# Performance work log

Measured on AMD Instinct MI355X. Metric: run time of the kernel, lower is better.

Reference implementation:

```python
import jax, jax.numpy as jnp
import numpy as np

B, P, N, E, IN, HID, NL, MULT = 4, 8, 2000, 2000, 16, 128, 3, 4
LOGIT_CLIP = 10.0

def setup_inputs() -> dict:
    key = jax.random.key(0)
    ks = jax.random.split(key, 8)
    s = 0.05
    return {
        "node_features": jax.random.normal(ks[0], (B, P, N, IN), jnp.float32),
        "incidence": jax.random.uniform(ks[1], (B, N, E), jnp.float32),  # weighted incidence
        "W_in": s * jax.random.normal(ks[2], (IN, HID), jnp.float32),
        "edge_Ws": s * jax.random.normal(ks[3], (NL, HID, HID), jnp.float32),
        "node_Ws": s * jax.random.normal(ks[4], (NL, HID, HID), jnp.float32),
        "W1": s * jax.random.normal(ks[5], (HID, MULT * HID), jnp.float32),
        "W2": s * jax.random.normal(ks[6], (MULT * HID, HID), jnp.float32),
        "W_dec": s * jax.random.normal(ks[7], (HID, 1), jnp.float32),
    }

def reference(node_features, incidence, W_in, edge_Ws, node_Ws, W1, W2, W_dec):
    # node_features: [B,P,N,in]; incidence H: [B,N,E] (broadcast over P instead of torch's repeat)
    x = node_features @ W_in                                   # [B,P,N,h]
    H = incidence
    n_layers = edge_Ws.shape[0]
    for l in range(n_layers):
        # node -> hyperedge aggregation: H^T @ x
        e = jnp.einsum('bne,bpnd->bped', H, x)                 # [B,P,E,h]
        e = jax.nn.relu(e @ edge_Ws[l])
        # hyperedge -> node aggregation: H @ e
        x = jnp.einsum('bne,bped->bpnd', H, e)                 # [B,P,N,h]
        x = jax.nn.relu(x @ node_Ws[l])
    # MLP: Linear -> ReLU -> Linear (dropout = 0)
    h = jax.nn.relu(x @ W1) @ W2                               # [B,P,N,h]
    out = h @ W_dec                                            # [B,P,N,1]
    out = out / jnp.sqrt(jnp.asarray(W_in.shape[1], jnp.float32))
    out = LOGIT_CLIP * jnp.tanh(out)
    return out
```

## Files before the change

kernel.cpp:

```cpp
#include <hip/hip_runtime.h>
#include <hip/hip_bf16.h>


typedef __attribute__((ext_vector_type(8))) short bf16x8;
typedef __attribute__((ext_vector_type(4))) float f32x4;

#define GLL16(gp, lp) __builtin_amdgcn_global_load_lds(                      \
    (const __attribute__((address_space(1))) void*)(gp),                     \
    (__attribute__((address_space(3))) void*)(lp), 16, 0, 0)

__device__ __forceinline__ unsigned short f2bf(float v) {
  __hip_bfloat16 h = __float2bfloat16(v);
  return __builtin_bit_cast(unsigned short, h);
}
__device__ __forceinline__ float bf2f(unsigned short u) {
  unsigned int x = ((unsigned int)u) << 16;
  return __builtin_bit_cast(float, x);
}

__global__ void convH_k(const float* __restrict__ H,
                        unsigned short* __restrict__ Hb,
                        unsigned short* __restrict__ HTb) {
  int b  = blockIdx.z;
  int n0 = blockIdx.y * 32, e0 = blockIdx.x * 32;
  __shared__ float t[32][33];
  int tx = threadIdx.x & 31, ty = threadIdx.x >> 5;
  for (int r = ty; r < 32; r += 8) {
    int n = n0 + r, e = e0 + tx;
    float v = (n < 2000 && e < 2000) ? H[((long)b * 2000 + n) * 2000 + e] : 0.f;
    t[r][tx] = v;
    Hb[((long)b * 2048 + n) * 2048 + e] = f2bf(v);
  }
  __syncthreads();
  for (int r = ty; r < 32; r += 8) {
    HTb[((long)b * 2048 + (e0 + r)) * 2048 + (n0 + tx)] = f2bf(t[tx][r]);
  }
}

__global__ void transposeW_k(const float* __restrict__ src,
                             unsigned short* __restrict__ dst, int R, int C) {
  __shared__ float t[32][33];
  int c0 = blockIdx.x * 32, r0 = blockIdx.y * 32;
  int tx = threadIdx.x & 31, ty = threadIdx.x >> 5;
  for (int rr = ty; rr < 32; rr += 8) {
    int rI = r0 + rr, cI = c0 + tx;
    t[rr][tx] = (rI < R && cI < C) ? src[(long)rI * C + cI] : 0.f;
  }
  __syncthreads();
  for (int rr = ty; rr < 32; rr += 8) {
    int cO = c0 + rr, rO = r0 + tx;
    if (cO < C && rO < R) dst[(long)cO * R + rO] = f2bf(t[tx][rr]);
  }
}

__global__ __launch_bounds__(256) void x0_k(
    const float* __restrict__ nf, const float* __restrict__ Win,
    unsigned short* __restrict__ xb, unsigned short* __restrict__ xTb) {
  __shared__ float nfs[128][16];
  __shared__ float wins[2048];
  __shared__ unsigned short xt[128][136];

  int bp = blockIdx.y;
  int n0 = blockIdx.x * 128;
  int tid = threadIdx.x;

  {
    int r = tid >> 1, c = (tid & 1) * 8;
    int n = n0 + r;
    float4 v0 = make_float4(0.f, 0.f, 0.f, 0.f), v1 = v0;
    if (n < 2000) {
      const float* src = nf + ((long)bp * 2000 + n) * 16 + c;
      v0 = *(const float4*)src;
      v1 = *(const float4*)(src + 4);
    }
    *(float4*)&nfs[r][c]     = v0;
    *(float4*)&nfs[r][c + 4] = v1;
  }
  {
    int base = tid * 8;
    float4 a = *(const float4*)(Win + base);
    float4 b = *(const float4*)(Win + base + 4);
    *(float4*)&wins[base]     = a;
    *(float4*)&wins[base + 4] = b;
  }
  __syncthreads();

  int d = tid & 127, half = tid >> 7;
  float wcol[16];
#pragma unroll
  for (int k = 0; k < 16; k++) wcol[k] = wins[k * 128 + d];

  unsigned short* xtRow = xTb + ((long)bp * 128 + d) * 2048 + n0 + half * 64;
#pragma unroll
  for (int oct = 0; oct < 8; oct++) {
    bf16x8 pk;
#pragma unroll
    for (int j = 0; j < 8; j++) {
      int nl = half * 64 + oct * 8 + j;
      float v = 0.f;
#pragma unroll
      for (int k = 0; k < 16; k++) v += nfs[nl][k] * wcol[k];
      unsigned short bits = f2bf(v);
      pk[j] = (short)bits;
      xt[nl][d] = bits;
    }
    *(bf16x8*)(xtRow + oct * 8) = pk;
  }
  __syncthreads();

  {
    int r = tid >> 1, c0 = (tid & 1) * 64;
    unsigned short* dst = xb + ((long)bp * 2048 + n0 + r) * 128 + c0;
#pragma unroll
    for (int i = 0; i < 8; i++) {
      bf16x8 v = *(const bf16x8*)&xt[r][c0 + i * 8];
      *(bf16x8*)(dst + i * 8) = v;
    }
  }
}

__global__ void wfuse_k(const float* __restrict__ W2, const float* __restrict__ Wdec,
                        float* __restrict__ wf) {
  int i = blockIdx.x * 256 + threadIdx.x;
  if (i < 512) {
    float s = 0.f;
#pragma unroll 8
    for (int j = 0; j < 128; j++) s += W2[i * 128 + j] * Wdec[j];
    wf[i] = s;
  }
}

template <int WN, int WT>
__global__ __launch_bounds__(256, 2) void gemm_fused(
    const unsigned short* __restrict__ A, int lda, long strideA, int aDiv,
    const unsigned short* __restrict__ BT, int ldbt, long strideBT,
    const unsigned short* __restrict__ Wt,
    unsigned short* __restrict__ Cn, int ldc, long strideCn,
    unsigned short* __restrict__ Ct, int ldct, long strideCt, int K) {
  int wgid = blockIdx.x;
  int orig = (wgid & 7) * 64 + (wgid >> 3);
  int mblk = orig & 15;
  int bz   = orig >> 4;
  A  += (long)(bz / aDiv) * strideA;
  BT += (long)bz * strideBT;
  int m0 = mblk * 128;

  __shared__ unsigned short smem[32768];

  int tid  = threadIdx.x;
  int lane = tid & 63;
  int w    = tid >> 6;
  int wr   = w >> 1, wc = w & 1;
  int fr   = lane & 15;
  int fg   = lane >> 4;

  int srow   = tid >> 3;
  int schunk = ((tid & 7) ^ (srow & 7)) * 8;
  const unsigned short* Agp[4];
  const unsigned short* Bgp[4];
#pragma unroll
  for (int i = 0; i < 4; i++) {
    Agp[i] = A + (long)(m0 + i * 32 + srow) * lda + schunk;
    Bgp[i] = BT + (long)(i * 32 + srow) * ldbt + schunk;
  }

#define STAGE(sel, tk) do {                                                  \
    long _k = (long)(tk) * 64;                                               \
    _Pragma("unroll")                                                        \
    for (int i = 0; i < 4; i++)                                              \
      GLL16(Agp[i] + _k, smem + (sel) * 16384 + (i * 256 + tid) * 8);        \
    _Pragma("unroll")                                                        \
    for (int i = 0; i < 4; i++)                                              \
      GLL16(Bgp[i] + _k, smem + (sel) * 16384 + 8192 + (i * 256 + tid) * 8); \
  } while (0)

  f32x4 acc[4][4] = {};
  const int cOff0 = (fg ^ (fr & 7)) * 8;
  const int cOff1 = ((4 + fg) ^ (fr & 7)) * 8;

#define PHASE(Asp, Bsp, CO) do {                                             \
    bf16x8 af[4], bv[4];                                                     \
    _Pragma("unroll")                                                        \
    for (int m = 0; m < 4; m++)                                              \
      af[m] = *(const bf16x8*)&(Asp)[(wr * 64 + m * 16 + fr) * 64 + (CO)];   \
    _Pragma("unroll")                                                        \
    for (int n = 0; n < 4; n++)                                              \
      bv[n] = *(const bf16x8*)&(Bsp)[(wc * 64 + n * 16 + fr) * 64 + (CO)];   \
    __builtin_amdgcn_s_setprio(1);                                           \
    _Pragma("unroll")                                                        \
    for (int m = 0; m < 4; m++)                                              \
      _Pragma("unroll")                                                      \
      for (int n = 0; n < 4; n++)                                            \
        acc[m][n] = __builtin_amdgcn_mfma_f32_16x16x32_bf16(af[m], bv[n],    \
                                                            acc[m][n], 0, 0, 0); \
    __builtin_amdgcn_s_setprio(0);                                           \
  } while (0)

#define COMPUTE64(sel) do {                                                  \
    const unsigned short* As_ = smem + (sel) * 16384;                        \
    const unsigned short* Bs_ = As_ + 8192;                                  \
    PHASE(As_, Bs_, cOff0);                                                  \
    PHASE(As_, Bs_, cOff1);                                                  \
  } while (0)

#define VMW(n) asm volatile("s_waitcnt vmcnt(" #n ")" ::: "memory")
#define BARR __builtin_amdgcn_s_barrier()
#define SCH0 __builtin_amdgcn_sched_barrier(0)

  int nt2 = K >> 6;

  STAGE(0, 0);
  int t = 0;
  for (; t + 2 < nt2; t += 2) {
    STAGE(1, t + 1);
    VMW(8); BARR; SCH0;
    COMPUTE64(0);
    BARR;
    STAGE(0, t + 2);
    VMW(8); BARR; SCH0;
    COMPUTE64(1);
    BARR;
  }
  STAGE(1, nt2 - 1);
  VMW(8); BARR; SCH0;
  COMPUTE64(0);
  BARR;
  VMW(0); BARR; SCH0;
  COMPUTE64(1);
#undef STAGE
#undef COMPUTE64
#undef PHASE

  unsigned short* Gs = smem;
#pragma unroll
  for (int m = 0; m < 4; m++) {
#pragma unroll
    for (int n = 0; n < 4; n++) {
      int rowb = wr * 64 + m * 16 + fg * 4;
      int col  = wc * 64 + n * 16 + fr;
      int ch = col >> 3, ci = col & 7;
#pragma unroll
      for (int r = 0; r < 4; r++) {
        int row = rowb + r;
        Gs[row * 128 + ((ch ^ (row & 7)) * 8) + ci] = f2bf(acc[m][n][r]);
      }
    }
  }
  __syncthreads();

  f32x4 acc2[4][4] = {};
#pragma unroll
  for (int kk = 0; kk < 4; kk++) {
    bf16x8 a2[4], b2[4];
#pragma unroll
    for (int m = 0; m < 4; m++) {
      int row = wr * 64 + m * 16 + fr;
      int c = kk * 4 + fg;
      a2[m] = *(const bf16x8*)&Gs[row * 128 + ((c ^ (fr & 7)) * 8)];
    }
#pragma unroll
    for (int n = 0; n < 4; n++) {
      int row = wc * 64 + n * 16 + fr;
      b2[n] = *(const bf16x8*)&Wt[row * 128 + (kk * 4 + fg) * 8];
    }
#pragma unroll
    for (int m = 0; m < 4; m++)
#pragma unroll
      for (int n = 0; n < 4; n++)
        acc2[m][n] = __builtin_amdgcn_mfma_f32_16x16x32_bf16(a2[m], b2[n], acc2[m][n], 0, 0, 0);
  }

  if (WN) {
#pragma unroll
    for (int m = 0; m < 4; m++) {
#pragma unroll
      for (int n = 0; n < 4; n++) {
        int rowb = m0 + wr * 64 + m * 16 + fg * 4;
        int col  = wc * 64 + n * 16 + fr;
        unsigned short* p = Cn + bz * strideCn + (long)rowb * ldc + col;
        p[0]       = f2bf(fmaxf(acc2[m][n][0], 0.f));
        p[ldc]     = f2bf(fmaxf(acc2[m][n][1], 0.f));
        p[2 * ldc] = f2bf(fmaxf(acc2[m][n][2], 0.f));
        p[3 * ldc] = f2bf(fmaxf(acc2[m][n][3], 0.f));
      }
    }
  }

  if (WT) {
    __syncthreads();
    unsigned short* GsT = smem;
#pragma unroll
    for (int m = 0; m < 4; m++) {
#pragma unroll
      for (int n = 0; n < 4; n++) {
        int rowb = wr * 64 + m * 16 + fg * 4;
        int col  = wc * 64 + n * 16 + fr;
        int chunk = rowb >> 3;
        ushort4 pk;
        pk.x = f2bf(fmaxf(acc2[m][n][0], 0.f));
        pk.y = f2bf(fmaxf(acc2[m][n][1], 0.f));
        pk.z = f2bf(fmaxf(acc2[m][n][2], 0.f));
        pk.w = f2bf(fmaxf(acc2[m][n][3], 0.f));
        *(ushort4*)&GsT[col * 128 + ((chunk ^ (col & 7)) * 8) + (rowb & 7)] = pk;
      }
    }
    __syncthreads();
    unsigned short* CtB = Ct + bz * strideCt + m0;
#pragma unroll
    for (int i = 0; i < 8; i++) {
      int s = i * 256 + tid;
      int col = s >> 4, slot = s & 15;
      int l = slot ^ (col & 7);
      bf16x8 v = *(const bf16x8*)&GsT[col * 128 + slot * 8];
      *(bf16x8*)(CtB + (long)col * ldct + l * 8) = v;
    }
  }
}

__global__ __launch_bounds__(256) void mlp_k(
    const unsigned short* __restrict__ X,
    const unsigned short* __restrict__ W1T,
    const float* __restrict__ wf,
    float* __restrict__ out) {
  __shared__ unsigned short Xs[128 * 128];
  __shared__ unsigned short Bs[128 * 128];
  __shared__ float rowacc[128];

  int tid  = threadIdx.x;
  int lane = tid & 63;
  int w    = tid >> 6, wr = w >> 1, wc = w & 1;
  int fr   = lane & 15, fg = lane >> 4;
  long m0  = (long)blockIdx.x * 128;

#pragma unroll
  for (int i = 0; i < 8; i++) {
    int s = i * 256 + tid;
    int r = s >> 4, c = (s & 15) ^ (r & 7);
    GLL16(X + (m0 + r) * 128 + c * 8, (unsigned short*)Xs + s * 8);
  }
  if (tid < 128) rowacc[tid] = 0.f;

  float rs[4][4] = {};

  for (int nb = 0; nb < 4; nb++) {
#pragma unroll
    for (int i = 0; i < 8; i++) {
      int s = i * 256 + tid;
      int r = s >> 4, c = (s & 15) ^ (r & 7);
      GLL16(W1T + (long)(nb * 128 + r) * 128 + c * 8, (unsigned short*)Bs + s * 8);
    }
    __syncthreads();

    f32x4 acc[4][4] = {};
#pragma unroll
    for (int kk = 0; kk < 4; kk++) {
      bf16x8 a2[4], b2[4];
#pragma unroll
      for (int m = 0; m < 4; m++) {
        int row = wr * 64 + m * 16 + fr;
        int c = kk * 4 + fg;
        a2[m] = *(const bf16x8*)&Xs[row * 128 + ((c ^ (row & 7)) * 8)];
      }
#pragma unroll
      for (int n = 0; n < 4; n++) {
        int row = wc * 64 + n * 16 + fr;
        int c = kk * 4 + fg;
        b2[n] = *(const bf16x8*)&Bs[row * 128 + ((c ^ (row & 7)) * 8)];
      }
#pragma unroll
      for (int m = 0; m < 4; m++)
#pragma unroll
        for (int n = 0; n < 4; n++)
          acc[m][n] = __builtin_amdgcn_mfma_f32_16x16x32_bf16(a2[m], b2[n], acc[m][n], 0, 0, 0);
    }

#pragma unroll
    for (int n = 0; n < 4; n++) {
      float wv = wf[nb * 128 + wc * 64 + n * 16 + fr];
#pragma unroll
      for (int m = 0; m < 4; m++)
#pragma unroll
        for (int r = 0; r < 4; r++)
          rs[m][r] += fmaxf(acc[m][n][r], 0.f) * wv;
    }
    __syncthreads();
  }

#pragma unroll
  for (int m = 0; m < 4; m++)
#pragma unroll
    for (int r = 0; r < 4; r++) {
      float v = rs[m][r];
      v += __shfl_xor(v, 1, 64);
      v += __shfl_xor(v, 2, 64);
      v += __shfl_xor(v, 4, 64);
      v += __shfl_xor(v, 8, 64);
      if (fr == 0) atomicAdd(&rowacc[wr * 64 + m * 16 + fg * 4 + r], v);
    }
  __syncthreads();

  if (tid < 128) {
    long row = m0 + tid;
    int bp = (int)(row >> 11), n = (int)(row & 2047);
    if (n < 2000)
      out[(long)bp * 2000 + n] = 10.f * tanhf(rowacc[tid] * 0.08838834764831843f);
  }
}

extern "C" void kernel_launch(void* const* d_in, const int* in_sizes, int n_in,
                              void* d_out, int out_size, void* d_ws, size_t ws_size,
                              hipStream_t stream) {
  const float* nf    = (const float*)d_in[0];
  const float* H     = (const float*)d_in[1];
  const float* Win   = (const float*)d_in[2];
  const float* edgeW = (const float*)d_in[3];
  const float* nodeW = (const float*)d_in[4];
  const float* W1    = (const float*)d_in[5];
  const float* W2    = (const float*)d_in[6];
  const float* Wdec  = (const float*)d_in[7];
  float* out = (float*)d_out;

  char* ws = (char*)d_ws;
  unsigned short* Hb   = (unsigned short*)(ws + 0);
  unsigned short* HTb  = (unsigned short*)(ws + 33554432);
  unsigned short* xb   = (unsigned short*)(ws + 67108864);
  unsigned short* xTb  = (unsigned short*)(ws + 83886080);
  unsigned short* eTb  = (unsigned short*)(ws + 100663296);
  unsigned short* edgeWT = (unsigned short*)(ws + 117440512);
  unsigned short* nodeWT = (unsigned short*)(ws + 117538816);
  unsigned short* W1T    = (unsigned short*)(ws + 117637120);
  float*          wf     = (float*)(ws + 117768192);
  (void)ws_size; (void)in_sizes; (void)n_in; (void)out_size;

  convH_k<<<dim3(64, 64, 4), 256, 0, stream>>>(H, Hb, HTb);
  for (int l = 0; l < 3; l++) {
    transposeW_k<<<dim3(4, 4), 256, 0, stream>>>(edgeW + l * 16384, edgeWT + l * 16384, 128, 128);
    transposeW_k<<<dim3(4, 4), 256, 0, stream>>>(nodeW + l * 16384, nodeWT + l * 16384, 128, 128);
  }
  transposeW_k<<<dim3(16, 4), 256, 0, stream>>>(W1, W1T, 128, 512);
  wfuse_k<<<2, 256, 0, stream>>>(W2, Wdec, wf);
  x0_k<<<dim3(16, 32), 256, 0, stream>>>(nf, Win, xb, xTb);

  for (int l = 0; l < 3; l++) {
    gemm_fused<0, 1><<<dim3(512), 256, 0, stream>>>(
        HTb, 2048, 2048L * 2048, 8, xTb, 2048, 128L * 2048,
        edgeWT + l * 16384,
        nullptr, 0, 0, eTb, 2048, 128L * 2048, 2048);
    if (l < 2) {
      gemm_fused<0, 1><<<dim3(512), 256, 0, stream>>>(
          Hb, 2048, 2048L * 2048, 8, eTb, 2048, 128L * 2048,
          nodeWT + l * 16384,
          nullptr, 0, 0, xTb, 2048, 128L * 2048, 2048);
    } else {
      gemm_fused<1, 1><<<dim3(512), 256, 0, stream>>>(
          Hb, 2048, 2048L * 2048, 8, eTb, 2048, 128L * 2048,
          nodeWT + l * 16384,
          xb, 128, 2048L * 128, xTb, 2048, 128L * 2048, 2048);
    }
  }

  mlp_k<<<dim3(512), 256, 0, stream>>>(xb, W1T, wf, out);
}
```

Measured before the change: 313.8 us.

## Widen GEMM tiles to cover two P slices, sharing each H tile

Restructures the fused hypergraph GEMM so each workgroup computes a 128x256 output spanning two P slices, loading each incidence tile once for both. The K step shrinks to 32 with a new LDS swizzle, and the grid halves. The x0 kernel also stops writing the unused row-major x copy. This cuts redundant H traffic but doubles accumulator registers per thread and leaves only one workgroup per CU, which risks spills and lower latency hiding.

```diff
diff --git a/kernel.cpp b/kernel.cpp
--- a/kernel.cpp
+++ b/kernel.cpp
@@ -55,10 +55,9 @@
 
 __global__ __launch_bounds__(256) void x0_k(
     const float* __restrict__ nf, const float* __restrict__ Win,
-    unsigned short* __restrict__ xb, unsigned short* __restrict__ xTb) {
+    unsigned short* __restrict__ xTb) {
   __shared__ float nfs[128][16];
   __shared__ float wins[2048];
-  __shared__ unsigned short xt[128][136];
 
   int bp = blockIdx.y;
   int n0 = blockIdx.x * 128;
@@ -90,7 +89,7 @@
 #pragma unroll
   for (int k = 0; k < 16; k++) wcol[k] = wins[k * 128 + d];
 
-  unsigned short* xtRow = xTb + ((long)bp * 128 + d) * 2048 + n0 + half * 64;
+  unsigned short* dst = xTb + ((long)bp * 128 + d) * 2048 + n0 + half * 64;
 #pragma unroll
   for (int oct = 0; oct < 8; oct++) {
     bf16x8 pk;
@@ -100,22 +99,9 @@
       float v = 0.f;
 #pragma unroll
       for (int k = 0; k < 16; k++) v += nfs[nl][k] * wcol[k];
-      unsigned short bits = f2bf(v);
-      pk[j] = (short)bits;
-      xt[nl][d] = bits;
-    }
-    *(bf16x8*)(xtRow + oct * 8) = pk;
-  }
-  __syncthreads();
-
-  {
-    int r = tid >> 1, c0 = (tid & 1) * 64;
-    unsigned short* dst = xb + ((long)bp * 2048 + n0 + r) * 128 + c0;
-#pragma unroll
-    for (int i = 0; i < 8; i++) {
-      bf16x8 v = *(const bf16x8*)&xt[r][c0 + i * 8];
-      *(bf16x8*)(dst + i * 8) = v;
-    }
+      pk[j] = (short)f2bf(v);
+    }
+    *(bf16x8*)(dst + oct * 8) = pk;
   }
 }
 
@@ -132,18 +118,21 @@
 
 template <int WN, int WT>
 __global__ __launch_bounds__(256, 2) void gemm_fused(
-    const unsigned short* __restrict__ A, int lda, long strideA, int aDiv,
-    const unsigned short* __restrict__ BT, int ldbt, long strideBT,
+    const unsigned short* __restrict__ A, int lda, long strideA,
+    const unsigned short* __restrict__ BT, long strideBT,
     const unsigned short* __restrict__ Wt,
     unsigned short* __restrict__ Cn, int ldc, long strideCn,
     unsigned short* __restrict__ Ct, int ldct, long strideCt, int K) {
   int wgid = blockIdx.x;
-  int orig = (wgid & 7) * 64 + (wgid >> 3);
+  int orig = (wgid & 7) * 32 + (wgid >> 3);
   int mblk = orig & 15;
-  int bz   = orig >> 4;
-  A  += (long)(bz / aDiv) * strideA;
-  BT += (long)bz * strideBT;
-  int m0 = mblk * 128;
+  int rest = orig >> 4;
+  int ntl  = rest & 3;
+  int b    = rest >> 2;
+  int m0   = mblk * 128;
+  int bp0  = b * 8 + ntl * 2;
+  A += (long)b * strideA;
+  const unsigned short* BTb = BT + (long)bp0 * strideBT;
 
   __shared__ unsigned short smem[32768];
 
@@ -154,119 +143,116 @@
   int fr   = lane & 15;
   int fg   = lane >> 4;
 
-  int srow   = tid >> 3;
-  int schunk = ((tid & 7) ^ (srow & 7)) * 8;
-  const unsigned short* Agp[4];
+  const unsigned short* Agp[2];
   const unsigned short* Bgp[4];
 #pragma unroll
+  for (int i = 0; i < 2; i++) {
+    int s = i * 256 + tid, row = s >> 2, gc = (s & 3) ^ ((row >> 1) & 3);
+    Agp[i] = A + (long)(m0 + row) * lda + gc * 8;
+  }
+#pragma unroll
   for (int i = 0; i < 4; i++) {
-    Agp[i] = A + (long)(m0 + i * 32 + srow) * lda + schunk;
-    Bgp[i] = BT + (long)(i * 32 + srow) * ldbt + schunk;
+    int s = i * 256 + tid, row = s >> 2, gc = (s & 3) ^ ((row >> 1) & 3);
+    Bgp[i] = BTb + (long)row * 2048 + gc * 8;
   }
 
 #define STAGE(sel, tk) do {                                                  \
-    long _k = (long)(tk) * 64;                                               \
+    int _k = (tk) * 32;                                                      \
+    _Pragma("unroll")                                                        \
+    for (int i = 0; i < 2; i++)                                              \
+      GLL16(Agp[i] + _k, smem + (sel) * 12288 + (i * 256 + tid) * 8);        \
     _Pragma("unroll")                                                        \
     for (int i = 0; i < 4; i++)                                              \
-      GLL16(Agp[i] + _k, smem + (sel) * 16384 + (i * 256 + tid) * 8);        \
-    _Pragma("unroll")                                                        \
-    for (int i = 0; i < 4; i++)                                              \
-      GLL16(Bgp[i] + _k, smem + (sel) * 16384 + 8192 + (i * 256 + tid) * 8); \
+      GLL16(Bgp[i] + _k, smem + (sel) * 12288 + 4096 + (i * 256 + tid) * 8); \
   } while (0)
 
-  f32x4 acc[4][4] = {};
-  const int cOff0 = (fg ^ (fr & 7)) * 8;
-  const int cOff1 = ((4 + fg) ^ (fr & 7)) * 8;
-
-#define PHASE(Asp, Bsp, CO) do {                                             \
-    bf16x8 af[4], bv[4];                                                     \
+  f32x4 acc[4][8] = {};
+  const int cIdx = (fg ^ ((fr >> 1) & 3)) * 8;
+
+#define COMPUTE(sel) do {                                                    \
+    const unsigned short* As_ = smem + (sel) * 12288;                        \
+    const unsigned short* Bs_ = As_ + 4096;                                  \
+    bf16x8 af[4], bv[8];                                                     \
     _Pragma("unroll")                                                        \
     for (int m = 0; m < 4; m++)                                              \
-      af[m] = *(const bf16x8*)&(Asp)[(wr * 64 + m * 16 + fr) * 64 + (CO)];   \
+      af[m] = *(const bf16x8*)&As_[(wr * 64 + m * 16 + fr) * 32 + cIdx];     \
     _Pragma("unroll")                                                        \
-    for (int n = 0; n < 4; n++)                                              \
-      bv[n] = *(const bf16x8*)&(Bsp)[(wc * 64 + n * 16 + fr) * 64 + (CO)];   \
+    for (int n = 0; n < 8; n++)                                              \
+      bv[n] = *(const bf16x8*)&Bs_[(wc * 128 + n * 16 + fr) * 32 + cIdx];    \
     __builtin_amdgcn_s_setprio(1);                                           \
     _Pragma("unroll")                                                        \
     for (int m = 0; m < 4; m++)                                              \
       _Pragma("unroll")                                                      \
-      for (int n = 0; n < 4; n++)                                            \
+      for (int n = 0; n < 8; n++)                                            \
         acc[m][n] = __builtin_amdgcn_mfma_f32_16x16x32_bf16(af[m], bv[n],    \
                                                             acc[m][n], 0, 0, 0); \
     __builtin_amdgcn_s_setprio(0);                                           \
   } while (0)
 
-#define COMPUTE64(sel) do {                                                  \
-    const unsigned short* As_ = smem + (sel) * 16384;                        \
-    const unsigned short* Bs_ = As_ + 8192;                                  \
-    PHASE(As_, Bs_, cOff0);                                                  \
-    PHASE(As_, Bs_, cOff1);                                                  \
-  } while (0)
-
 #define VMW(n) asm volatile("s_waitcnt vmcnt(" #n ")" ::: "memory")
 #define BARR __builtin_amdgcn_s_barrier()
 #define SCH0 __builtin_amdgcn_sched_barrier(0)
 
-  int nt2 = K >> 6;
+  int nt = K >> 5;
 
   STAGE(0, 0);
   int t = 0;
-  for (; t + 2 < nt2; t += 2) {
+  for (; t + 2 < nt; t += 2) {
     STAGE(1, t + 1);
-    VMW(8); BARR; SCH0;
-    COMPUTE64(0);
+    VMW(6); BARR; SCH0;
+    COMPUTE(0);
     BARR;
     STAGE(0, t + 2);
-    VMW(8); BARR; SCH0;
-    COMPUTE64(1);
+    VMW(6); BARR; SCH0;
+    COMPUTE(1);
     BARR;
   }
-  STAGE(1, nt2 - 1);
-  VMW(8); BARR; SCH0;
-  COMPUTE64(0);
+  STAGE(1, nt - 1);
+  VMW(6); BARR; SCH0;
+  COMPUTE(0);
   BARR;
   VMW(0); BARR; SCH0;
-  COMPUTE64(1);
+  COMPUTE(1);
 #undef STAGE
-#undef COMPUTE64
-#undef PHASE
+#undef COMPUTE
+  __syncthreads();
 
   unsigned short* Gs = smem;
 #pragma unroll
   for (int m = 0; m < 4; m++) {
 #pragma unroll
-    for (int n = 0; n < 4; n++) {
+    for (int n = 0; n < 8; n++) {
       int rowb = wr * 64 + m * 16 + fg * 4;
-      int col  = wc * 64 + n * 16 + fr;
+      int col  = wc * 128 + n * 16 + fr;
       int ch = col >> 3, ci = col & 7;
 #pragma unroll
       for (int r = 0; r < 4; r++) {
         int row = rowb + r;
-        Gs[row * 128 + ((ch ^ (row & 7)) * 8) + ci] = f2bf(acc[m][n][r]);
+        Gs[row * 256 + ((ch ^ (row & 7)) * 8) + ci] = f2bf(acc[m][n][r]);
       }
     }
   }
   __syncthreads();
 
-  f32x4 acc2[4][4] = {};
+  f32x4 acc2[4][8] = {};
 #pragma unroll
   for (int kk = 0; kk < 4; kk++) {
-    bf16x8 a2[4], b2[4];
+    bf16x8 a2[4], b2[8];
 #pragma unroll
     for (int m = 0; m < 4; m++) {
       int row = wr * 64 + m * 16 + fr;
-      int c = kk * 4 + fg;
-      a2[m] = *(const bf16x8*)&Gs[row * 128 + ((c ^ (fr & 7)) * 8)];
-    }
-#pragma unroll
-    for (int n = 0; n < 4; n++) {
-      int row = wc * 64 + n * 16 + fr;
+      int ch = wc * 16 + kk * 4 + fg;
+      a2[m] = *(const bf16x8*)&Gs[row * 256 + ((ch ^ (row & 7)) * 8)];
+    }
+#pragma unroll
+    for (int n = 0; n < 8; n++) {
+      int row = n * 16 + fr;
       b2[n] = *(const bf16x8*)&Wt[row * 128 + (kk * 4 + fg) * 8];
     }
 #pragma unroll
     for (int m = 0; m < 4; m++)
 #pragma unroll
-      for (int n = 0; n < 4; n++)
+      for (int n = 0; n < 8; n++)
         acc2[m][n] = __builtin_amdgcn_mfma_f32_16x16x32_bf16(a2[m], b2[n], acc2[m][n], 0, 0, 0);
   }
 
@@ -274,10 +260,10 @@
 #pragma unroll
     for (int m = 0; m < 4; m++) {
 #pragma unroll
-      for (int n = 0; n < 4; n++) {
+      for (int n = 0; n < 8; n++) {
         int rowb = m0 + wr * 64 + m * 16 + fg * 4;
-        int col  = wc * 64 + n * 16 + fr;
-        unsigned short* p = Cn + bz * strideCn + (long)rowb * ldc + col;
+        int col  = n * 16 + fr;
+        unsigned short* p = Cn + (bp0 + wc) * strideCn + (long)rowb * ldc + col;
         p[0]       = f2bf(fmaxf(acc2[m][n][0], 0.f));
         p[ldc]     = f2bf(fmaxf(acc2[m][n][1], 0.f));
         p[2 * ldc] = f2bf(fmaxf(acc2[m][n][2], 0.f));
@@ -292,27 +278,26 @@
 #pragma unroll
     for (int m = 0; m < 4; m++) {
 #pragma unroll
-      for (int n = 0; n < 4; n++) {
+      for (int n = 0; n < 8; n++) {
         int rowb = wr * 64 + m * 16 + fg * 4;
-        int col  = wc * 64 + n * 16 + fr;
-        int chunk = rowb >> 3;
+        int col  = n * 16 + fr;
+        int slot = (rowb >> 3) ^ (col & 7);
         ushort4 pk;
         pk.x = f2bf(fmaxf(acc2[m][n][0], 0.f));
         pk.y = f2bf(fmaxf(acc2[m][n][1], 0.f));
         pk.z = f2bf(fmaxf(acc2[m][n][2], 0.f));
         pk.w = f2bf(fmaxf(acc2[m][n][3], 0.f));
-        *(ushort4*)&GsT[col * 128 + ((chunk ^ (col & 7)) * 8) + (rowb & 7)] = pk;
+        *(ushort4*)&GsT[wc * 16384 + col * 128 + slot * 8 + (rowb & 7)] = pk;
       }
     }
     __syncthreads();
-    unsigned short* CtB = Ct + bz * strideCt + m0;
-#pragma unroll
-    for (int i = 0; i < 8; i++) {
+#pragma unroll
+    for (int i = 0; i < 16; i++) {
       int s = i * 256 + tid;
-      int col = s >> 4, slot = s & 15;
+      int pI = s >> 11, col = (s >> 4) & 127, slot = s & 15;
       int l = slot ^ (col & 7);
-      bf16x8 v = *(const bf16x8*)&GsT[col * 128 + slot * 8];
-      *(bf16x8*)(CtB + (long)col * ldct + l * 8) = v;
+      bf16x8 v = *(const bf16x8*)&GsT[pI * 16384 + col * 128 + slot * 8];
+      *(bf16x8*)(Ct + (bp0 + pI) * strideCt + (long)col * ldct + m0 + l * 8) = v;
     }
   }
 }
@@ -439,21 +424,21 @@
   }
   transposeW_k<<<dim3(16, 4), 256, 0, stream>>>(W1, W1T, 128, 512);
   wfuse_k<<<2, 256, 0, stream>>>(W2, Wdec, wf);
-  x0_k<<<dim3(16, 32), 256, 0, stream>>>(nf, Win, xb, xTb);
+  x0_k<<<dim3(16, 32), 256, 0, stream>>>(nf, Win, xTb);
 
   for (int l = 0; l < 3; l++) {
-    gemm_fused<0, 1><<<dim3(512), 256, 0, stream>>>(
-        HTb, 2048, 2048L * 2048, 8, xTb, 2048, 128L * 2048,
+    gemm_fused<0, 1><<<dim3(256), 256, 0, stream>>>(
+        HTb, 2048, 2048L * 2048, xTb, 128L * 2048,
         edgeWT + l * 16384,
         nullptr, 0, 0, eTb, 2048, 128L * 2048, 2048);
     if (l < 2) {
-      gemm_fused<0, 1><<<dim3(512), 256, 0, stream>>>(
-          Hb, 2048, 2048L * 2048, 8, eTb, 2048, 128L * 2048,
+      gemm_fused<0, 1><<<dim3(256), 256, 0, stream>>>(
+          Hb, 2048, 2048L * 2048, eTb, 128L * 2048,
           nodeWT + l * 16384,
           nullptr, 0, 0, xTb, 2048, 128L * 2048, 2048);
     } else {
-      gemm_fused<1, 1><<<dim3(512), 256, 0, stream>>>(
-          Hb, 2048, 2048L * 2048, 8, eTb, 2048, 128L * 2048,
+      gemm_fused<1, 1><<<dim3(256), 256, 0, stream>>>(
+          Hb, 2048, 2048L * 2048, eTb, 128L * 2048,
           nodeWT + l * 16384,
           xb, 128, 2048L * 128, xTb, 2048, 128L * 2048, 2048);
     }
```

Result: slower. 364.7 us (+16.2%).
